# Kernel tuning notes

Hardware: AMD Instinct MI355X
Metric: run time of the kernel (lower is better)

## Reference

```python
import jax, jax.numpy as jnp
import numpy as np

N, D_IN, R, D_OUT, U = 500000, 128, 256, 64, 10000
EPS = 1e-8


def _vb_layer(m, v, W_mu, W_lv, relu_out):
    # Variational Bayes linear layer, moment propagation:
    #   out_mean = m @ W_mu
    #   out_var  = v @ (W_mu^2 + W_var) + m^2 @ W_var,  W_var = exp(W_lv)
    W_var = jnp.exp(W_lv)
    M = m @ W_mu
    V = v @ (W_mu * W_mu + W_var) + (m * m) @ W_var
    if relu_out:
        gate = (M > 0).astype(M.dtype)
        M = M * gate
        V = V * gate
    return M, V


def setup_inputs() -> dict:
    key = jax.random.key(0)
    ks = jax.random.split(key, 6)
    X = jax.random.normal(ks[0], (N, D_IN), jnp.float32)
    X_idx = jnp.sort(jax.random.randint(ks[1], (N,), 0, U, dtype=jnp.int32))
    W_mu0 = jax.random.normal(ks[2], (D_IN, R), jnp.float32) / np.sqrt(D_IN)
    W_lv0 = jax.random.normal(ks[3], (D_IN, R), jnp.float32) * 0.1 - 4.0
    W_mu1 = jax.random.normal(ks[4], (R, D_OUT), jnp.float32) / np.sqrt(R)
    W_lv1 = jax.random.normal(ks[5], (R, D_OUT), jnp.float32) * 0.1 - 4.0
    return {"X": X, "X_idx": X_idx, "W_mu0": W_mu0, "W_lv0": W_lv0,
            "W_mu1": W_mu1, "W_lv1": W_lv1}


def reference(X, X_idx, W_mu0, W_lv0, W_mu1, W_lv1):
    m, v = _vb_layer(X, jnp.zeros_like(X), W_mu0, W_lv0, True)   # [N, R]
    m, v = _vb_layer(m, v, W_mu1, W_lv1, False)                  # [N, D_OUT]
    v = jnp.maximum(v, EPS)
    inv_v = 1.0 / v
    # precision-weighted aggregation per group id (replaces per-uid loop)
    var_inv_sum = jax.ops.segment_sum(inv_v, X_idx, num_segments=U) + EPS
    mean_sum = jax.ops.segment_sum(m * inv_v, X_idx, num_segments=U)
    emb_var = 1.0 / var_inv_sum          # [U, D_OUT]
    emb_mean = mean_sum * emb_var        # [U, D_OUT]
    return emb_mean, emb_var
```

## Files before the change

### kernel.cpp

```cpp
#include <hip/hip_runtime.h>
#include <stdint.h>

#define N_ROWS 500000
#define U_DIM 10000
#define EPSV 1e-8f
#define NT16 31250

typedef __attribute__((ext_vector_type(8))) short bf16x8;
typedef __attribute__((ext_vector_type(4))) float f32x4;

__device__ __forceinline__ short f2bf(float f) {
  unsigned u = __float_as_uint(f);
  u += 0x7fffu + ((u >> 16) & 1u);
  return (short)(u >> 16);
}
__device__ __forceinline__ float bf2f(short s) {
  return __uint_as_float(((unsigned)(unsigned short)s) << 16);
}

__global__ void prep_weights(const float* __restrict__ Wmu0,
                             const float* __restrict__ Wlv0,
                             const float* __restrict__ Wmu1,
                             const float* __restrict__ Wlv1,
                             short* __restrict__ wgt) {
  int i = blockIdx.x * blockDim.x + threadIdx.x;
  if (i < 32768) {
    int c = i & 255, k = i >> 8;
    int rc = c >> 5, ct = (c >> 4) & 1, n = c & 15;
    int kt = k >> 5, q = (k >> 3) & 3, u = k & 7;
    int lane = q * 16 + n;
    float mu = Wmu0[k * 256 + c];
    float ev = __expf(Wlv0[k * 256 + c]);
    wgt[((((rc * 2 + 0) * 2 + ct) * 4 + kt) * 64 + lane) * 8 + u] = f2bf(mu);
    wgt[((((rc * 2 + 1) * 2 + ct) * 4 + kt) * 64 + lane) * 8 + u] = f2bf(ev);
  } else if (i < 49152) {
    int i2 = i - 32768;
    int o = i2 & 63, j = i2 >> 6;
    int rc = j >> 5, q = (j >> 3) & 3, u = j & 7;
    int ct1 = o >> 4, n = o & 15;
    int lane = q * 16 + n;
    float mu = Wmu1[j * 64 + o];
    float ev = __expf(Wlv1[j * 64 + o]);
    int b = 65536 + (((rc * 4 + ct1) * 3 + 0) * 64 + lane) * 8 + u;
    wgt[b]        = f2bf(mu);
    wgt[b + 512]  = f2bf(mu * mu + ev);
    wgt[b + 1024] = f2bf(ev);
  }
}

__global__ __launch_bounds__(256, 4) void vb_fused(
    const float* __restrict__ X, const int* __restrict__ Xidx,
    const short* __restrict__ wgt, float* __restrict__ out) {
  __shared__ __align__(16) short stage[2][8192];
  __shared__ __align__(16) short ldsM[4][512];
  __shared__ __align__(16) short ldsV[4][512];

  const int tid  = threadIdx.x;
  const int w    = tid >> 6;
  const int lane = tid & 63;
  const int n    = lane & 15;
  const int q    = lane >> 4;
  const int T    = blockIdx.x * 4 + w;
  const bool active = (T < NT16);
  const int row0 = active ? T * 16 : (N_ROWS - 16);

  const f32x4 zf4 = {0.f, 0.f, 0.f, 0.f};
  const int lane8 = lane * 8;

  bf16x8 a_m[4], a_sq[4];
  {
    const float* xr = X + (size_t)(row0 + n) * 128;
#pragma unroll
    for (int kt = 0; kt < 4; ++kt) {
      float xf[8];
      *(float4*)&xf[0] = *(const float4*)&xr[kt * 32 + q * 8];
      *(float4*)&xf[4] = *(const float4*)&xr[kt * 32 + q * 8 + 4];
#pragma unroll
      for (int u = 0; u < 8; ++u) {
        a_m[kt][u]  = f2bf(xf[u]);
        a_sq[kt][u] = f2bf(xf[u] * xf[u]);
      }
    }
  }

  f32x4 accm1[4], accv1[4];
#pragma unroll
  for (int c = 0; c < 4; ++c) { accm1[c] = zf4; accv1[c] = zf4; }

  const char* gbase = (const char*)wgt;
#define ISSUE_STAGE(rc_, buf_)                                                 \
  do {                                                                         \
    _Pragma("unroll")                                                          \
    for (int s_ = 0; s_ < 4; ++s_) {                                           \
      __builtin_amdgcn_global_load_lds(                                        \
          (const __attribute__((address_space(1))) unsigned int*)              \
              (gbase + (rc_) * 16384 + s_ * 4096 + tid * 16),                  \
          (__attribute__((address_space(3))) unsigned int*)                    \
              ((char*)&stage[buf_][0] + s_ * 4096 + (w << 10)),                \
          16, 0, 0);                                                           \
    }                                                                          \
  } while (0)

  ISSUE_STAGE(0, 0);

#pragma unroll
  for (int rc = 0; rc < 8; ++rc) {
    __syncthreads();
    if (rc < 7) ISSUE_STAGE(rc + 1, (rc + 1) & 1);

    const short* st = &stage[rc & 1][0];

    f32x4 accm0[2], accv0[2];
    accm0[0] = zf4; accm0[1] = zf4; accv0[0] = zf4; accv0[1] = zf4;
#pragma unroll
    for (int kt = 0; kt < 4; ++kt) {
#pragma unroll
      for (int ct = 0; ct < 2; ++ct) {
        bf16x8 bm = *(const bf16x8*)&st[((0 * 2 + ct) * 4 + kt) * 512 + lane8];
        bf16x8 bv = *(const bf16x8*)&st[((1 * 2 + ct) * 4 + kt) * 512 + lane8];
        accm0[ct] = __builtin_amdgcn_mfma_f32_16x16x32_bf16(a_m[kt],  bm, accm0[ct], 0, 0, 0);
        accv0[ct] = __builtin_amdgcn_mfma_f32_16x16x32_bf16(a_sq[kt], bv, accv0[ct], 0, 0, 0);
      }
    }

#pragma unroll
    for (int ct = 0; ct < 2; ++ct) {
      const int csw = (ct * 16 + n) ^ (q << 3);
#pragma unroll
      for (int reg = 0; reg < 4; ++reg) {
        float m = accm0[ct][reg], v = accv0[ct][reg];
        if (!(m > 0.f)) { m = 0.f; v = 0.f; }
        const int row = q * 4 + reg;
        ldsM[w][row * 32 + csw] = f2bf(m);
        ldsV[w][row * 32 + csw] = f2bf(v);
      }
    }
    const int roff = n * 32 + (((q ^ (n >> 2)) & 3) << 3);
    bf16x8 am = *(const bf16x8*)&ldsM[w][roff];
    bf16x8 av = *(const bf16x8*)&ldsV[w][roff];
    bf16x8 asq;
#pragma unroll
    for (int u = 0; u < 8; ++u) {
      float f = bf2f(am[u]);
      asq[u] = f2bf(f * f);
    }

    const short* l1b = wgt + 65536 + rc * 6144 + lane8;
#pragma unroll
    for (int ct1 = 0; ct1 < 4; ++ct1) {
      const short* fb = l1b + ct1 * 1536;
      bf16x8 b1 = *(const bf16x8*)&fb[0];
      bf16x8 b2 = *(const bf16x8*)&fb[512];
      bf16x8 b3 = *(const bf16x8*)&fb[1024];
      accm1[ct1] = __builtin_amdgcn_mfma_f32_16x16x32_bf16(am,  b1, accm1[ct1], 0, 0, 0);
      accv1[ct1] = __builtin_amdgcn_mfma_f32_16x16x32_bf16(av,  b2, accv1[ct1], 0, 0, 0);
      accv1[ct1] = __builtin_amdgcn_mfma_f32_16x16x32_bf16(asq, b3, accv1[ct1], 0, 0, 0);
    }
  }
#undef ISSUE_STAGE

  if (!active) return;
  float* meanp = out;
  float* varp  = out + U_DIM * 64;
  int4 idx4 = *(const int4*)&Xidx[row0 + q * 4];
  int uid[4] = {idx4.x, idx4.y, idx4.z, idx4.w};
#pragma unroll
  for (int ct = 0; ct < 4; ++ct) {
    const int o = ct * 16 + n;
    float sm = 0.f, sv = 0.f;
    int cur = uid[0];
#pragma unroll
    for (int reg = 0; reg < 4; ++reg) {
      float v1 = fmaxf(accv1[ct][reg], EPSV);
      float inv = 1.0f / v1;
      float mi  = accm1[ct][reg] * inv;
      if (uid[reg] != cur) {
        atomicAdd(&meanp[cur * 64 + o], sm);
        atomicAdd(&varp[cur * 64 + o], sv);
        sm = 0.f; sv = 0.f; cur = uid[reg];
      }
      sm += mi; sv += inv;
    }
    atomicAdd(&meanp[cur * 64 + o], sm);
    atomicAdd(&varp[cur * 64 + o], sv);
  }
}

__global__ void finalize(float* __restrict__ out) {
  int i = blockIdx.x * blockDim.x + threadIdx.x;
  if (i < U_DIM * 64) {
    float s = out[U_DIM * 64 + i];
    float var = 1.0f / (s + EPSV);
    out[U_DIM * 64 + i] = var;
    out[i] = out[i] * var;
  }
}

extern "C" void kernel_launch(void* const* d_in, const int* in_sizes, int n_in,
                              void* d_out, int out_size, void* d_ws, size_t ws_size,
                              hipStream_t stream) {
  (void)in_sizes; (void)n_in; (void)out_size; (void)ws_size;
  const float* X    = (const float*)d_in[0];
  const int*   Xidx = (const int*)d_in[1];
  const float* Wmu0 = (const float*)d_in[2];
  const float* Wlv0 = (const float*)d_in[3];
  const float* Wmu1 = (const float*)d_in[4];
  const float* Wlv1 = (const float*)d_in[5];
  float* out = (float*)d_out;
  short* wgt = (short*)d_ws;

  hipMemsetAsync(d_out, 0, (size_t)U_DIM * 64 * 2 * sizeof(float), stream);
  prep_weights<<<192, 256, 0, stream>>>(Wmu0, Wlv0, Wmu1, Wlv1, wgt);
  vb_fused<<<7813, 256, 0, stream>>>(X, Xidx, wgt, out);
  finalize<<<(U_DIM * 64 + 255) / 256, 256, 0, stream>>>(out);
}
```

Baseline: 553.1 us.

## Swap MFMA operands so layer-0 output feeds layer-1 from registers without LDS

Layer-0 MFMAs now take their operands in swapped order, so each lane's accumulator holds a transposed tile. The ReLU-gated mean and variance can then be packed directly into the bf16 A-operands for layer 1, with no LDS round trip. The layer-1 weight prepack permutes its K ordering to match the new register-to-K mapping. This removes the per-chunk LDS writes, reads and bank traffic, and it also squares m in fp32 before rounding rather than squaring an already-rounded bf16 value.

```diff
diff --git a/kernel.cpp b/kernel.cpp
--- a/kernel.cpp
+++ b/kernel.cpp
@@ -13,9 +13,6 @@
   unsigned u = __float_as_uint(f);
   u += 0x7fffu + ((u >> 16) & 1u);
   return (short)(u >> 16);
-}
-__device__ __forceinline__ float bf2f(short s) {
-  return __uint_as_float(((unsigned)(unsigned short)s) << 16);
 }
 
 __global__ void prep_weights(const float* __restrict__ Wmu0,
@@ -36,7 +33,9 @@
   } else if (i < 49152) {
     int i2 = i - 32768;
     int o = i2 & 63, j = i2 >> 6;
-    int rc = j >> 5, q = (j >> 3) & 3, u = j & 7;
+    int rc = j >> 5, jl = j & 31;
+    int q = (jl >> 2) & 3;
+    int u = ((jl >> 4) << 2) | (jl & 3);
     int ct1 = o >> 4, n = o & 15;
     int lane = q * 16 + n;
     float mu = Wmu1[j * 64 + o];
@@ -52,8 +51,6 @@
     const float* __restrict__ X, const int* __restrict__ Xidx,
     const short* __restrict__ wgt, float* __restrict__ out) {
   __shared__ __align__(16) short stage[2][8192];
-  __shared__ __align__(16) short ldsM[4][512];
-  __shared__ __align__(16) short ldsV[4][512];
 
   const int tid  = threadIdx.x;
   const int w    = tid >> 6;
@@ -118,31 +115,20 @@
       for (int ct = 0; ct < 2; ++ct) {
         bf16x8 bm = *(const bf16x8*)&st[((0 * 2 + ct) * 4 + kt) * 512 + lane8];
         bf16x8 bv = *(const bf16x8*)&st[((1 * 2 + ct) * 4 + kt) * 512 + lane8];
-        accm0[ct] = __builtin_amdgcn_mfma_f32_16x16x32_bf16(a_m[kt],  bm, accm0[ct], 0, 0, 0);
-        accv0[ct] = __builtin_amdgcn_mfma_f32_16x16x32_bf16(a_sq[kt], bv, accv0[ct], 0, 0, 0);
+        accm0[ct] = __builtin_amdgcn_mfma_f32_16x16x32_bf16(bm, a_m[kt],  accm0[ct], 0, 0, 0);
+        accv0[ct] = __builtin_amdgcn_mfma_f32_16x16x32_bf16(bv, a_sq[kt], accv0[ct], 0, 0, 0);
       }
     }
 
-#pragma unroll
-    for (int ct = 0; ct < 2; ++ct) {
-      const int csw = (ct * 16 + n) ^ (q << 3);
-#pragma unroll
-      for (int reg = 0; reg < 4; ++reg) {
-        float m = accm0[ct][reg], v = accv0[ct][reg];
-        if (!(m > 0.f)) { m = 0.f; v = 0.f; }
-        const int row = q * 4 + reg;
-        ldsM[w][row * 32 + csw] = f2bf(m);
-        ldsV[w][row * 32 + csw] = f2bf(v);
-      }
-    }
-    const int roff = n * 32 + (((q ^ (n >> 2)) & 3) << 3);
-    bf16x8 am = *(const bf16x8*)&ldsM[w][roff];
-    bf16x8 av = *(const bf16x8*)&ldsV[w][roff];
-    bf16x8 asq;
+    bf16x8 am, av, asq;
 #pragma unroll
     for (int u = 0; u < 8; ++u) {
-      float f = bf2f(am[u]);
-      asq[u] = f2bf(f * f);
+      float m = accm0[u >> 2][u & 3];
+      float v = accv0[u >> 2][u & 3];
+      if (!(m > 0.f)) { m = 0.f; v = 0.f; }
+      am[u]  = f2bf(m);
+      av[u]  = f2bf(v);
+      asq[u] = f2bf(m * m);
     }
 
     const short* l1b = wgt + 65536 + rc * 6144 + lane8;
```

Measured after the change: 584.3 us. 1.06x slower.
